# Kernel tuning notes

Measured on AMD Instinct MI355X. Metric: run time of the kernel, lower is better.

## Reference

```python
import jax, jax.numpy as jnp
import numpy as np

K_EDE = 10.0   # self.k
T_EDE = 0.1    # self.t
BN_EPS = 1e-5
T_A = 576.0    # 3*3*64, hardcoded in my_bn1/my_bn2


def qfn(x, prec):
    # dorefa-style round quantizer with straight-through gradient
    n = float(2 ** prec - 1)
    return x + jax.lax.stop_gradient(jnp.round(x * n) / n - x)


@jax.custom_vjp
def binary_quantize(x):
    return jnp.sign(x)


def _bq_fwd(x):
    return jnp.sign(x), x


def _bq_bwd(x, g):
    # IR-Net EDE backward: k * t * (1 - tanh(x*t)^2)
    return (K_EDE * T_EDE * (1.0 - jnp.tanh(x * T_EDE) ** 2) * g,)


binary_quantize.defvjp(_bq_fwd, _bq_bwd)


def _clip_T(x):
    T = jnp.maximum(jnp.abs(x.min()), jnp.abs(x.max()))
    return jax.lax.stop_gradient(jnp.clip(T, 1e-10, 255.0))


def quantize_conv_act(x, prec):
    # my_quantize_conv: clamp to [-T, T], scale to [-1,1], qfn (no rescale by T)
    T = _clip_T(x)
    return qfn(jnp.clip(x, -T, T) / T, prec)


def quantize(x, prec):
    # my_quantize: same but rescaled back by T
    T = _clip_T(x)
    return qfn(jnp.clip(x, -T, T) / T, prec) * T


def ir_conv2d(a, w, stride):
    # IR-Net 1w8a IRConv2d: per-out-channel normalize, binarize (sign), power-of-2 scale
    co = w.shape[0]
    wf = w.reshape(co, -1)
    bw = (w - wf.mean(1)[:, None, None, None]) / jnp.std(wf, axis=1, ddof=1)[:, None, None, None]
    sw = jax.lax.stop_gradient(
        2.0 ** jnp.round(jnp.log2(jnp.abs(bw.reshape(co, -1)).mean(1)))
    )[:, None, None, None]
    bw = binary_quantize(bw) * sw
    return jax.lax.conv_general_dilated(
        a, bw, window_strides=(stride, stride), padding=[(1, 1), (1, 1)],
        dimension_numbers=('NCHW', 'OIHW', 'NCHW'))


def bn_as_quantized_affine(x, gamma, beta, mean, var):
    # my_bn1/my_bn2 (eval mode): BN folded into per-channel scale+bias.
    # The original builds a CxC diagonal 1x1 conv; since off-diagonal entries are 0,
    # both the quantization stats (max|.|) and the conv reduce exactly to this
    # per-channel affine, which is the faithful fused form.
    std = jnp.sqrt(var + BN_EPS)
    w = gamma / std
    b = beta - w * mean
    qw = quantize(w, 3)
    qb = quantize(b, 12)
    aq = qfn(x / T_A, 10) * T_A  # my_quantize_activation(input, 10, T_a)
    return aq * qw[None, :, None, None] + qb[None, :, None, None]


def _block(x, w1, w2, g1, b1, m1, v1, g2, b2, m2, v2):
    xq = quantize_conv_act(x, 3)
    out = ir_conv2d(xq, w1, 1)
    out = bn_as_quantized_affine(out, g1, b1, m1, v1) + xq  # identity shortcut
    out = jnp.clip(out, -1.0, 1.0)  # hardtanh
    x1 = quantize_conv_act(out, 3)
    out = ir_conv2d(x1, w2, 1)
    out = bn_as_quantized_affine(out, g2, b2, m2, v2) + x1
    return jnp.clip(out, -1.0, 1.0)


def setup_inputs() -> dict:
    key = jax.random.key(0)
    ks = jax.random.split(key, 11)
    B, C, H, W = 128, 64, 56, 56
    return {
        'x': jax.random.normal(ks[0], (B, C, H, W), jnp.float32),
        'w1': jax.random.normal(ks[1], (C, C, 3, 3), jnp.float32) * 0.1,
        'w2': jax.random.normal(ks[2], (C, C, 3, 3), jnp.float32) * 0.1,
        'g1': jax.random.uniform(ks[3], (C,), jnp.float32, 0.5, 1.5),
        'b1': jax.random.normal(ks[4], (C,), jnp.float32) * 0.1,
        'm1': jax.random.normal(ks[5], (C,), jnp.float32) * 0.1,
        'v1': jax.random.uniform(ks[6], (C,), jnp.float32, 0.5, 1.5),
        'g2': jax.random.uniform(ks[7], (C,), jnp.float32, 0.5, 1.5),
        'b2': jax.random.normal(ks[8], (C,), jnp.float32) * 0.1,
        'm2': jax.random.normal(ks[9], (C,), jnp.float32) * 0.1,
        'v2': jax.random.uniform(ks[10], (C,), jnp.float32, 0.5, 1.5),
    }


def reference(x, w1, w2, g1, b1, m1, v1, g2, b2, m2, v2):
    return _block(x, w1, w2, g1, b1, m1, v1, g2, b2, m2, v2)
```

## Files before the change

kernel.cpp:

```cpp
#include <hip/hip_runtime.h>
#include <stdint.h>

typedef int v4i   __attribute__((ext_vector_type(4)));
typedef int v16i  __attribute__((ext_vector_type(16)));

#define B_    128
#define C_    64
#define H_    56
#define W_    56
#define HW_   3136
#define NELEM (B_*C_*HW_)

#define OFF_K0   0
#define OFF_K1   ((size_t)NELEM)
#define OFF_WB   ((size_t)2*NELEM)
#define OFF_PAR  (OFF_WB + 2*9*64*64)
#define OFF_MAX  (OFF_PAR + 384*4)

__global__ void k_absmax(const float* __restrict__ x, unsigned* __restrict__ maxbits) {
    __shared__ float smax[4];
    float m = 0.f;
    const int n4 = NELEM / 4;
    for (int i = blockIdx.x * blockDim.x + threadIdx.x; i < n4; i += gridDim.x * blockDim.x) {
        float4 v = ((const float4*)x)[i];
        m = fmaxf(m, fmaxf(fmaxf(fabsf(v.x), fabsf(v.y)), fmaxf(fabsf(v.z), fabsf(v.w))));
    }
    for (int off = 32; off; off >>= 1) m = fmaxf(m, __shfl_down(m, off, 64));
    if ((threadIdx.x & 63) == 0) smax[threadIdx.x >> 6] = m;
    __syncthreads();
    if (threadIdx.x == 0) {
        float mm = fmaxf(fmaxf(smax[0], smax[1]), fmaxf(smax[2], smax[3]));
        atomicMax(maxbits, __float_as_uint(mm));
    }
}

__global__ void k_quant(const float* __restrict__ x, const unsigned* __restrict__ maxbits,
                        int8_t* __restrict__ k8) {
    __shared__ __align__(16) int8_t tile[W_ * C_];
    const int n = blockIdx.x / H_;
    const int y = blockIdx.x % H_;
    const float T = fminf(fmaxf(__uint_as_float(*maxbits), 1e-10f), 255.0f);
    for (int i = threadIdx.x; i < C_ * 14; i += blockDim.x) {
        int c = i / 14, j = i % 14;
        float4 v = *(const float4*)(x + ((size_t)(n * C_ + c)) * HW_ + y * W_ + j * 4);
        float vv[4] = {v.x, v.y, v.z, v.w};
#pragma unroll
        for (int q = 0; q < 4; q++) {
            float t = fminf(fmaxf(vv[q], -T), T);
            float u = __fdiv_rn(t, T);
            int k = (int)rintf(__fmul_rn(u, 7.0f));
            tile[(j * 4 + q) * C_ + c] = (int8_t)k;
        }
    }
    __syncthreads();
    int4* dst = (int4*)(k8 + ((size_t)(n * H_ + y)) * W_ * C_);
    for (int i = threadIdx.x; i < W_ * C_ / 16; i += blockDim.x)
        dst[i] = ((const int4*)tile)[i];
}

__device__ __forceinline__ float pw_reduce64(float r) {
    r = __fadd_rn(r, __shfl_xor(r, 1, 64));
    r = __fadd_rn(r, __shfl_xor(r, 2, 64));
    r = __fadd_rn(r, __shfl_xor(r, 4, 64));
    r = __fadd_rn(r, __shfl_xor(r, 8, 64));
    r = __fadd_rn(r, __shfl_xor(r, 16, 64));
    r = __fadd_rn(r, __shfl_xor(r, 32, 64));
    return r;
}

__global__ void k_prepw(const float* __restrict__ w1, const float* __restrict__ w2,
                        int8_t* __restrict__ wb, float* __restrict__ par) {
    const int layer = blockIdx.x >> 6;
    const int co    = blockIdx.x & 63;
    const float* w = (layer ? w2 : w1) + (size_t)co * 576;
    const int lane = threadIdx.x;
    const int base = (lane >> 3) * 72 + (lane & 7);

    float v[9];
#pragma unroll
    for (int i = 0; i < 9; i++) v[i] = w[base + 8 * i];

    float s = v[0];
#pragma unroll
    for (int i = 1; i < 9; i++) s = __fadd_rn(s, v[i]);
    const float mean = __fdiv_rn(pw_reduce64(s), 576.0f);

    float d0 = __fsub_rn(v[0], mean);
    float sq = __fmul_rn(d0, d0);
#pragma unroll
    for (int i = 1; i < 9; i++) {
        float d = __fsub_rn(v[i], mean);
        sq = __fadd_rn(sq, __fmul_rn(d, d));
    }
    const float sig = __fsqrt_rn(__fdiv_rn(pw_reduce64(sq), 575.0f));

    float sa = fabsf(__fdiv_rn(__fsub_rn(v[0], mean), sig));
#pragma unroll
    for (int i = 1; i < 9; i++)
        sa = __fadd_rn(sa, fabsf(__fdiv_rn(__fsub_rn(v[i], mean), sig)));
    const float ma = __fdiv_rn(pw_reduce64(sa), 576.0f);
    const float p  = rintf(log2f(ma));
    if (lane == 0) par[256 + layer * 64 + co] = __fdiv_rn(exp2f(p), 7.0f);

#pragma unroll
    for (int i = 0; i < 9; i++) {
        int ig = base + 8 * i;
        float d = __fsub_rn(v[i], mean);
        int8_t sg = (d > 0.0f) ? (int8_t)1 : ((d < 0.0f) ? (int8_t)-1 : (int8_t)0);
        int ci = ig / 9, t = ig % 9;
        wb[(((size_t)layer * 9 + t) * 64 + co) * 64 + ci] = sg;
    }
}

__global__ void k_prepbn(const float* g1, const float* bb1, const float* mm1, const float* vv1,
                         const float* g2, const float* bb2, const float* mm2, const float* vv2,
                         float* __restrict__ par) {
    const int layer = threadIdx.x >> 6;
    const int c = threadIdx.x & 63;
    const float* g  = layer ? g2  : g1;
    const float* be = layer ? bb2 : bb1;
    const float* mu = layer ? mm2 : mm1;
    const float* va = layer ? vv2 : vv1;
    const float stdv = __fsqrt_rn(__fadd_rn(va[c], 1e-5f));
    const float w = __fdiv_rn(g[c], stdv);
    const float b = __fsub_rn(be[c], __fmul_rn(w, mu[c]));
    float aw = fabsf(w), ab = fabsf(b);
    for (int off = 32; off; off >>= 1) {
        aw = fmaxf(aw, __shfl_xor(aw, off, 64));
        ab = fmaxf(ab, __shfl_xor(ab, off, 64));
    }
    const float Tw = fminf(fmaxf(aw, 1e-10f), 255.0f);
    const float Tb = fminf(fmaxf(ab, 1e-10f), 255.0f);
    {
        float vq = __fdiv_rn(fminf(fmaxf(w, -Tw), Tw), Tw);
        float r  = rintf(__fmul_rn(vq, 7.0f));
        float qf = __fadd_rn(vq, __fsub_rn(__fdiv_rn(r, 7.0f), vq));
        par[layer * 64 + c] = __fmul_rn(qf, Tw);
    }
    {
        float vq = __fdiv_rn(fminf(fmaxf(b, -Tb), Tb), Tb);
        float r  = rintf(__fmul_rn(vq, 4095.0f));
        float qf = __fadd_rn(vq, __fsub_rn(__fdiv_rn(r, 4095.0f), vq));
        par[128 + layer * 64 + c] = __fmul_rn(qf, Tb);
    }
}

template <int LAYER>
__global__ __launch_bounds__(256) void k_conv(const int8_t* __restrict__ kin,
                                              const int8_t* __restrict__ wb,
                                              const float* __restrict__ par,
                                              int8_t* __restrict__ kout,
                                              float* __restrict__ fout) {
    __shared__ __align__(16) int8_t halo[4 * 58 * 64];
    __shared__ __align__(16) int8_t wsm[9 * 64 * 64];
    const int n  = blockIdx.x / 28;
    const int y0 = (blockIdx.x % 28) * 2;
    const int tid = threadIdx.x;

    for (int u = tid; u < 928; u += 256) {
        int r = u / 232, rem = u % 232;
        int cp = rem / 4, part = rem % 4;
        int y = y0 - 1 + r, xg = cp - 1;
        int4 val = {0, 0, 0, 0};
        if (y >= 0 && y < 56 && xg >= 0 && xg < 56)
            val = *(const int4*)(kin + (((size_t)(n * 56 + y)) * 56 + xg) * 64 + part * 16);
        *(int4*)(halo + u * 16) = val;
    }
    const int8_t* wsrc = wb + (size_t)(LAYER - 1) * 9 * 64 * 64;
    for (int u = tid; u < 2304; u += 256)
        *(int4*)(wsm + u * 16) = *(const int4*)(wsrc + u * 16);
    __syncthreads();

    const int wv = tid >> 6, lane = tid & 63;
    const int mbase = wv * 32;
    const int ml = lane & 31;
    const int khalf = lane >> 5;
    const int m = mbase + ml;
    const int m_eff = (m < 112) ? m : 111;
    const int rm = m_eff / 56, cm = m_eff % 56;

    v16i acc0, acc1;
#pragma unroll
    for (int i = 0; i < 16; i++) { acc0[i] = 0; acc1[i] = 0; }

#pragma unroll
    for (int s = 0; s < 9; s++) {
        const int ky = s / 3, kx = s % 3;
        const int abase  = ((rm + ky) * 58 + (cm + kx)) * 64 + khalf * 16;
        const int bbase0 = (s * 64 + ml) * 64 + khalf * 16;
        const int bbase1 = (s * 64 + 32 + ml) * 64 + khalf * 16;
#pragma unroll
        for (int kb = 0; kb < 2; kb++) {
            v4i a  = *(const v4i*)(halo + abase  + kb * 32);
            v4i b0 = *(const v4i*)(wsm  + bbase0 + kb * 32);
            v4i b1 = *(const v4i*)(wsm  + bbase1 + kb * 32);
            acc0 = __builtin_amdgcn_mfma_i32_32x32x32_i8(a, b0, acc0, 0, 0, 0);
            acc1 = __builtin_amdgcn_mfma_i32_32x32x32_i8(a, b1, acc1, 0, 0, 0);
        }
    }
    __syncthreads();

    const float* qw = par + (LAYER - 1) * 64;
    const float* qb = par + 128 + (LAYER - 1) * 64;
    const float* sc = par + 256 + (LAYER - 1) * 64;
#pragma unroll
    for (int t = 0; t < 2; t++) {
        const int co = ml + t * 32;
        const float qwf = qw[co], qbf = qb[co], scf = sc[co];
#pragma unroll
        for (int r = 0; r < 16; r++) {
            const int mrow = mbase + (r & 3) + 8 * (r >> 2) + 4 * khalf;
            if (mrow >= 112) continue;
            const float Sf = (float)(t ? acc1[r] : acc0[r]);
            float convf = __fmul_rn(Sf, scf);
            float xb = __fdiv_rn(convf, 576.0f);
            float rr = rintf(__fmul_rn(xb, 1023.0f));
            float q1 = __fdiv_rn(rr, 1023.0f);
            float y1 = __fadd_rn(xb, __fsub_rn(q1, xb));
            float aq = __fmul_rn(y1, 576.0f);
            const int rloc = mrow / 56, cloc = mrow % 56;
            float kcf = (float)halo[((rloc + 1) * 58 + (cloc + 1)) * 64 + co];
            float xqv = __fdiv_rn(kcf, 7.0f);
            float val = __fadd_rn(__fadd_rn(__fmul_rn(aq, qwf), qbf), xqv);
            val = fminf(fmaxf(val, -1.0f), 1.0f);
            if (LAYER == 1) {
                int k2 = (int)rintf(__fmul_rn(val, 7.0f));
                wsm[mrow * 64 + co] = (int8_t)k2;
            } else {
                *(float*)&wsm[((size_t)co * 112 + mrow) * 4] = val;
            }
        }
    }
    __syncthreads();

    const size_t posbase = (size_t)n * HW_ + (size_t)y0 * 56;
    if (LAYER == 1) {
        int4* dst = (int4*)(kout + posbase * 64);
        for (int u = tid; u < 448; u += 256) dst[u] = ((const int4*)wsm)[u];
    } else {
        for (int u = tid; u < 1792; u += 256) {
            int co = u / 28, q = u % 28;
            float4 v = *((const float4*)wsm + co * 28 + q);
            *(float4*)(fout + ((size_t)(n * 64 + co)) * HW_ + (size_t)y0 * 56 + q * 4) = v;
        }
    }
}

extern "C" void kernel_launch(void* const* d_in, const int* in_sizes, int n_in,
                              void* d_out, int out_size, void* d_ws, size_t ws_size,
                              hipStream_t stream) {
    const float* x  = (const float*)d_in[0];
    const float* w1 = (const float*)d_in[1];
    const float* w2 = (const float*)d_in[2];
    const float* g1 = (const float*)d_in[3];
    const float* b1 = (const float*)d_in[4];
    const float* m1 = (const float*)d_in[5];
    const float* v1 = (const float*)d_in[6];
    const float* g2 = (const float*)d_in[7];
    const float* b2 = (const float*)d_in[8];
    const float* m2 = (const float*)d_in[9];
    const float* v2 = (const float*)d_in[10];

    char* ws = (char*)d_ws;
    int8_t*  k0  = (int8_t*)(ws + OFF_K0);
    int8_t*  k1  = (int8_t*)(ws + OFF_K1);
    int8_t*  wbp = (int8_t*)(ws + OFF_WB);
    float*   par = (float*)(ws + OFF_PAR);
    unsigned* mx = (unsigned*)(ws + OFF_MAX);

    hipMemsetAsync(mx, 0, 4, stream);
    k_absmax<<<1024, 256, 0, stream>>>(x, mx);
    k_quant<<<B_ * H_, 256, 0, stream>>>(x, mx, k0);
    k_prepw<<<128, 64, 0, stream>>>(w1, w2, wbp, par);
    k_prepbn<<<1, 128, 0, stream>>>(g1, b1, m1, v1, g2, b2, m2, v2, par);
    k_conv<1><<<B_ * 28, 256, 0, stream>>>(k0, wbp, par, k1, nullptr);
    k_conv<2><<<B_ * 28, 256, 0, stream>>>(k1, wbp, par, nullptr, (float*)d_out);
}
```

Before: 350.0 us.

## Tile conv over four rows with channel-group layout and LUT-based requant epilogue

```diff
diff --git a/kernel.cpp b/kernel.cpp
--- a/kernel.cpp
+++ b/kernel.cpp
@@ -14,8 +14,8 @@
 #define OFF_K0   0
 #define OFF_K1   ((size_t)NELEM)
 #define OFF_WB   ((size_t)2*NELEM)
-#define OFF_PAR  (OFF_WB + 2*9*64*64)
-#define OFF_MAX  (OFF_PAR + 384*4)
+#define OFF_PAR  (OFF_WB + 2*4*9*64*16)
+#define OFF_MAX  (OFF_PAR + 6144)
 
 __global__ void k_absmax(const float* __restrict__ x, unsigned* __restrict__ maxbits) {
     __shared__ float smax[4];
@@ -53,9 +53,11 @@
         }
     }
     __syncthreads();
-    int4* dst = (int4*)(k8 + ((size_t)(n * H_ + y)) * W_ * C_);
-    for (int i = threadIdx.x; i < W_ * C_ / 16; i += blockDim.x)
-        dst[i] = ((const int4*)tile)[i];
+    if (threadIdx.x < 224) {
+        int g = threadIdx.x / 56, xx = threadIdx.x % 56;
+        *(int4*)(k8 + ((((size_t)(n * 56 + y)) * 4 + g) * 56 + xx) * 16) =
+            *(const int4*)(tile + xx * 64 + g * 16);
+    }
 }
 
 __device__ __forceinline__ float pw_reduce64(float r) {
@@ -100,7 +102,8 @@
         sa = __fadd_rn(sa, fabsf(__fdiv_rn(__fsub_rn(v[i], mean), sig)));
     const float ma = __fdiv_rn(pw_reduce64(sa), 576.0f);
     const float p  = rintf(log2f(ma));
-    if (lane == 0) par[256 + layer * 64 + co] = __fdiv_rn(exp2f(p), 7.0f);
+    if (lane == 0)
+        ((double*)(par + 1280))[layer * 64 + co] = exp2((double)p) * (341.0 / 1344.0);
 
 #pragma unroll
     for (int i = 0; i < 9; i++) {
@@ -108,41 +111,46 @@
         float d = __fsub_rn(v[i], mean);
         int8_t sg = (d > 0.0f) ? (int8_t)1 : ((d < 0.0f) ? (int8_t)-1 : (int8_t)0);
         int ci = ig / 9, t = ig % 9;
-        wb[(((size_t)layer * 9 + t) * 64 + co) * 64 + ci] = sg;
+        wb[((((size_t)layer * 4 + (ci >> 4)) * 9 + t) * 64 + co) * 16 + (ci & 15)] = sg;
     }
 }
 
 __global__ void k_prepbn(const float* g1, const float* bb1, const float* mm1, const float* vv1,
                          const float* g2, const float* bb2, const float* mm2, const float* vv2,
                          float* __restrict__ par) {
-    const int layer = threadIdx.x >> 6;
-    const int c = threadIdx.x & 63;
-    const float* g  = layer ? g2  : g1;
-    const float* be = layer ? bb2 : bb1;
-    const float* mu = layer ? mm2 : mm1;
-    const float* va = layer ? vv2 : vv1;
-    const float stdv = __fsqrt_rn(__fadd_rn(va[c], 1e-5f));
-    const float w = __fdiv_rn(g[c], stdv);
-    const float b = __fsub_rn(be[c], __fmul_rn(w, mu[c]));
-    float aw = fabsf(w), ab = fabsf(b);
-    for (int off = 32; off; off >>= 1) {
-        aw = fmaxf(aw, __shfl_xor(aw, off, 64));
-        ab = fmaxf(ab, __shfl_xor(ab, off, 64));
-    }
-    const float Tw = fminf(fmaxf(aw, 1e-10f), 255.0f);
-    const float Tb = fminf(fmaxf(ab, 1e-10f), 255.0f);
-    {
-        float vq = __fdiv_rn(fminf(fmaxf(w, -Tw), Tw), Tw);
-        float r  = rintf(__fmul_rn(vq, 7.0f));
-        float qf = __fadd_rn(vq, __fsub_rn(__fdiv_rn(r, 7.0f), vq));
-        par[layer * 64 + c] = __fmul_rn(qf, Tw);
-    }
-    {
-        float vq = __fdiv_rn(fminf(fmaxf(b, -Tb), Tb), Tb);
-        float r  = rintf(__fmul_rn(vq, 4095.0f));
-        float qf = __fadd_rn(vq, __fsub_rn(__fdiv_rn(r, 4095.0f), vq));
-        par[128 + layer * 64 + c] = __fmul_rn(qf, Tb);
-    }
+    const int tid = threadIdx.x;
+    if (tid < 128) {
+        const int layer = tid >> 6;
+        const int c = tid & 63;
+        const float* g  = layer ? g2  : g1;
+        const float* be = layer ? bb2 : bb1;
+        const float* mu = layer ? mm2 : mm1;
+        const float* va = layer ? vv2 : vv1;
+        const float stdv = __fsqrt_rn(__fadd_rn(va[c], 1e-5f));
+        const float w = __fdiv_rn(g[c], stdv);
+        const float b = __fsub_rn(be[c], __fmul_rn(w, mu[c]));
+        float aw = fabsf(w), ab = fabsf(b);
+        for (int off = 32; off; off >>= 1) {
+            aw = fmaxf(aw, __shfl_xor(aw, off, 64));
+            ab = fmaxf(ab, __shfl_xor(ab, off, 64));
+        }
+        const float Tw = fminf(fmaxf(aw, 1e-10f), 255.0f);
+        const float Tb = fminf(fmaxf(ab, 1e-10f), 255.0f);
+        {
+            float vq = __fdiv_rn(fminf(fmaxf(w, -Tw), Tw), Tw);
+            float r  = rintf(__fmul_rn(vq, 7.0f));
+            float qf = __fadd_rn(vq, __fsub_rn(__fdiv_rn(r, 7.0f), vq));
+            par[layer * 64 + c] = __fmul_rn(qf, Tw);
+        }
+        {
+            float vq = __fdiv_rn(fminf(fmaxf(b, -Tb), Tb), Tb);
+            float r  = rintf(__fmul_rn(vq, 4095.0f));
+            float qf = __fadd_rn(vq, __fsub_rn(__fdiv_rn(r, 4095.0f), vq));
+            par[128 + layer * 64 + c] = __fmul_rn(qf, Tb);
+        }
+    }
+    for (int i = tid; i < 1024; i += blockDim.x)
+        par[256 + i] = __fmul_rn(__fdiv_rn((float)i, 1023.0f), 576.0f);
 }
 
 template <int LAYER>
@@ -151,97 +159,120 @@
                                               const float* __restrict__ par,
                                               int8_t* __restrict__ kout,
                                               float* __restrict__ fout) {
-    __shared__ __align__(16) int8_t halo[4 * 58 * 64];
-    __shared__ __align__(16) int8_t wsm[9 * 64 * 64];
-    const int n  = blockIdx.x / 28;
-    const int y0 = (blockIdx.x % 28) * 2;
+    constexpr int OUTB = (LAYER == 2) ? 57600 : 36864;
+    __shared__ __align__(16) int8_t smem[22272 + OUTB + 64];
+    int8_t* halo = smem;
+    int8_t* wsm  = smem + 22272;
+    float*  out2 = (float*)(smem + 22272);
+    float*  xqlut = (float*)(smem + 22272 + OUTB);
+
+    const int n  = blockIdx.x / 14;
+    const int y0 = (blockIdx.x % 14) * 4;
     const int tid = threadIdx.x;
 
-    for (int u = tid; u < 928; u += 256) {
-        int r = u / 232, rem = u % 232;
-        int cp = rem / 4, part = rem % 4;
-        int y = y0 - 1 + r, xg = cp - 1;
+    for (int u = tid; u < 1392; u += 256) {
+        int xx = u % 58, gr = u / 58;
+        int g = gr / 6, r = gr % 6;
+        int y = y0 - 1 + r, xg = xx - 1;
         int4 val = {0, 0, 0, 0};
         if (y >= 0 && y < 56 && xg >= 0 && xg < 56)
-            val = *(const int4*)(kin + (((size_t)(n * 56 + y)) * 56 + xg) * 64 + part * 16);
-        *(int4*)(halo + u * 16) = val;
-    }
-    const int8_t* wsrc = wb + (size_t)(LAYER - 1) * 9 * 64 * 64;
+            val = *(const int4*)(kin + ((((size_t)(n * 56 + y)) * 4 + g) * 56 + xg) * 16);
+        *(int4*)(halo + ((g * 6 + r) * 58 + xx) * 16) = val;
+    }
+    const int8_t* wsrc = wb + (size_t)(LAYER - 1) * 36864;
     for (int u = tid; u < 2304; u += 256)
         *(int4*)(wsm + u * 16) = *(const int4*)(wsrc + u * 16);
+    if (tid < 15) xqlut[tid] = __fdiv_rn((float)(tid - 7), 7.0f);
     __syncthreads();
 
     const int wv = tid >> 6, lane = tid & 63;
-    const int mbase = wv * 32;
-    const int ml = lane & 31;
-    const int khalf = lane >> 5;
-    const int m = mbase + ml;
-    const int m_eff = (m < 112) ? m : 111;
-    const int rm = m_eff / 56, cm = m_eff % 56;
-
-    v16i acc0, acc1;
-#pragma unroll
-    for (int i = 0; i < 16; i++) { acc0[i] = 0; acc1[i] = 0; }
+    const int ml = lane & 31, khalf = lane >> 5;
+    const int wvbase = wv * 64;
+
+    int rmT[2], cmT[2];
+#pragma unroll
+    for (int T = 0; T < 2; T++) {
+        int m = wvbase + T * 32 + ml;
+        if (m > 223) m = 223;
+        int q = (m * 586) >> 15;
+        rmT[T] = q; cmT[T] = m - q * 56;
+    }
+
+    v16i acc[2][2];
+#pragma unroll
+    for (int a = 0; a < 2; a++)
+#pragma unroll
+        for (int b = 0; b < 2; b++)
+#pragma unroll
+            for (int i = 0; i < 16; i++) acc[a][b][i] = 0;
 
 #pragma unroll
     for (int s = 0; s < 9; s++) {
         const int ky = s / 3, kx = s % 3;
-        const int abase  = ((rm + ky) * 58 + (cm + kx)) * 64 + khalf * 16;
-        const int bbase0 = (s * 64 + ml) * 64 + khalf * 16;
-        const int bbase1 = (s * 64 + 32 + ml) * 64 + khalf * 16;
 #pragma unroll
         for (int kb = 0; kb < 2; kb++) {
-            v4i a  = *(const v4i*)(halo + abase  + kb * 32);
-            v4i b0 = *(const v4i*)(wsm  + bbase0 + kb * 32);
-            v4i b1 = *(const v4i*)(wsm  + bbase1 + kb * 32);
-            acc0 = __builtin_amdgcn_mfma_i32_32x32x32_i8(a, b0, acc0, 0, 0, 0);
-            acc1 = __builtin_amdgcn_mfma_i32_32x32x32_i8(a, b1, acc1, 0, 0, 0);
-        }
-    }
-    __syncthreads();
-
-    const float* qw = par + (LAYER - 1) * 64;
-    const float* qb = par + 128 + (LAYER - 1) * 64;
-    const float* sc = par + 256 + (LAYER - 1) * 64;
+            const int g = kb * 2 + khalf;
+            v4i a0 = *(const v4i*)(halo + ((g * 6 + rmT[0] + ky) * 58 + cmT[0] + kx) * 16);
+            v4i a1 = *(const v4i*)(halo + ((g * 6 + rmT[1] + ky) * 58 + cmT[1] + kx) * 16);
+            v4i b0 = *(const v4i*)(wsm + ((g * 9 + s) * 64 + ml) * 16);
+            v4i b1 = *(const v4i*)(wsm + ((g * 9 + s) * 64 + ml + 32) * 16);
+            acc[0][0] = __builtin_amdgcn_mfma_i32_32x32x32_i8(a0, b0, acc[0][0], 0, 0, 0);
+            acc[0][1] = __builtin_amdgcn_mfma_i32_32x32x32_i8(a0, b1, acc[0][1], 0, 0, 0);
+            acc[1][0] = __builtin_amdgcn_mfma_i32_32x32x32_i8(a1, b0, acc[1][0], 0, 0, 0);
+            acc[1][1] = __builtin_amdgcn_mfma_i32_32x32x32_i8(a1, b1, acc[1][1], 0, 0, 0);
+        }
+    }
+
+    if (LAYER == 2) __syncthreads();
+
+    const float* qw  = par + (LAYER - 1) * 64;
+    const float* qb  = par + 128 + (LAYER - 1) * 64;
+    const float* aql = par + 256;
+    const double* Kd = (const double*)(par + 1280) + (LAYER - 1) * 64;
+
 #pragma unroll
     for (int t = 0; t < 2; t++) {
-        const int co = ml + t * 32;
-        const float qwf = qw[co], qbf = qb[co], scf = sc[co];
-#pragma unroll
-        for (int r = 0; r < 16; r++) {
-            const int mrow = mbase + (r & 3) + 8 * (r >> 2) + 4 * khalf;
-            if (mrow >= 112) continue;
-            const float Sf = (float)(t ? acc1[r] : acc0[r]);
-            float convf = __fmul_rn(Sf, scf);
-            float xb = __fdiv_rn(convf, 576.0f);
-            float rr = rintf(__fmul_rn(xb, 1023.0f));
-            float q1 = __fdiv_rn(rr, 1023.0f);
-            float y1 = __fadd_rn(xb, __fsub_rn(q1, xb));
-            float aq = __fmul_rn(y1, 576.0f);
-            const int rloc = mrow / 56, cloc = mrow % 56;
-            float kcf = (float)halo[((rloc + 1) * 58 + (cloc + 1)) * 64 + co];
-            float xqv = __fdiv_rn(kcf, 7.0f);
-            float val = __fadd_rn(__fadd_rn(__fmul_rn(aq, qwf), qbf), xqv);
-            val = fminf(fmaxf(val, -1.0f), 1.0f);
-            if (LAYER == 1) {
-                int k2 = (int)rintf(__fmul_rn(val, 7.0f));
-                wsm[mrow * 64 + co] = (int8_t)k2;
-            } else {
-                *(float*)&wsm[((size_t)co * 112 + mrow) * 4] = val;
+        const int co = ml + 32 * t;
+        const float qwf = qw[co], qbf = qb[co];
+        const double Kc = Kd[co];
+        const int hbase = (co >> 4) * 6;
+#pragma unroll
+        for (int T = 0; T < 2; T++) {
+#pragma unroll
+            for (int r = 0; r < 16; r++) {
+                const int mrow = wvbase + T * 32 + 4 * khalf + (r & 3) + 8 * (r >> 2);
+                if (mrow > 223) continue;
+                const int S = acc[T][t][r];
+                const int rri = (int)rint((double)S * Kc);
+                const int idx = rri < 0 ? -rri : rri;
+                float aqa = (idx <= 1023) ? aql[idx]
+                          : __fmul_rn(__fdiv_rn((float)idx, 1023.0f), 576.0f);
+                const float aq = rri < 0 ? -aqa : aqa;
+                const int rloc = (mrow * 586) >> 15;
+                const int cloc = mrow - rloc * 56;
+                const int kc = (int)halo[((hbase + rloc + 1) * 58 + cloc + 1) * 16 + (co & 15)];
+                const float xq = xqlut[kc + 7];
+                float val = __fadd_rn(__fadd_rn(__fmul_rn(aq, qwf), qbf), xq);
+                val = fminf(fmaxf(val, -1.0f), 1.0f);
+                if (LAYER == 1) {
+                    const int k2 = (int)rintf(__fmul_rn(val, 7.0f));
+                    const int y = y0 + rloc;
+                    kout[((((size_t)(n * 56 + y)) * 4 + (co >> 4)) * 56 + cloc) * 16 + (co & 15)]
+                        = (int8_t)k2;
+                } else {
+                    out2[co * 225 + mrow] = val;
+                }
             }
         }
     }
-    __syncthreads();
-
-    const size_t posbase = (size_t)n * HW_ + (size_t)y0 * 56;
-    if (LAYER == 1) {
-        int4* dst = (int4*)(kout + posbase * 64);
-        for (int u = tid; u < 448; u += 256) dst[u] = ((const int4*)wsm)[u];
-    } else {
-        for (int u = tid; u < 1792; u += 256) {
-            int co = u / 28, q = u % 28;
-            float4 v = *((const float4*)wsm + co * 28 + q);
-            *(float4*)(fout + ((size_t)(n * 64 + co)) * HW_ + (size_t)y0 * 56 + q * 4) = v;
+
+    if (LAYER == 2) {
+        __syncthreads();
+        float* dst = fout + (size_t)n * 64 * HW_ + (size_t)y0 * 56;
+        for (int it = 0; it < 56; it++) {
+            int u = it * 256 + tid;
+            int co = u / 224, m = u - co * 224;
+            dst[(size_t)co * HW_ + m] = out2[co * 225 + m];
         }
     }
 }
@@ -272,7 +303,7 @@
     k_absmax<<<1024, 256, 0, stream>>>(x, mx);
     k_quant<<<B_ * H_, 256, 0, stream>>>(x, mx, k0);
     k_prepw<<<128, 64, 0, stream>>>(w1, w2, wbp, par);
-    k_prepbn<<<1, 128, 0, stream>>>(g1, b1, m1, v1, g2, b2, m2, v2, par);
-    k_conv<1><<<B_ * 28, 256, 0, stream>>>(k0, wbp, par, k1, nullptr);
-    k_conv<2><<<B_ * 28, 256, 0, stream>>>(k1, wbp, par, nullptr, (float*)d_out);
-}
+    k_prepbn<<<1, 256, 0, stream>>>(g1, b1, m1, v1, g2, b2, m2, v2, par);
+    k_conv<1><<<B_ * 14, 256, 0, stream>>>(k0, wbp, par, k1, nullptr);
+    k_conv<2><<<B_ * 14, 256, 0, stream>>>(k1, wbp, par, nullptr, (float*)d_out);
+}
```

Result: slower. 398.8 us (+13.9%).
